# Kernel tuning notes

Hardware: AMD Instinct MI355X
Metric: run time of the kernel (lower is better)

Reference implementation:

```python
import jax, jax.numpy as jnp
import numpy as np

NX, NQ, NU, NY = 256, 256, 64, 64
EPS, ALPHA = 1e-3, 0.0
B = 32768


def setup_inputs() -> dict:
    key = jax.random.key(0)
    ks = jax.random.split(key, 8)
    std = np.float32(0.1 / np.sqrt(NX))
    return {
        "t": 0,
        "xi": jax.random.normal(ks[0], (B, NX), jnp.float32),
        "u": jax.random.normal(ks[1], (B, NU), jnp.float32),
        "Pstar": jax.random.normal(ks[2], (NX, NX), jnp.float32) * std,
        "Chi": jax.random.normal(ks[3], (NX, NQ), jnp.float32) * std,
        "Y1": jax.random.normal(ks[4], (NX, NX), jnp.float32) * std,
        "B2": jax.random.normal(ks[5], (NX, NU), jnp.float32) * std,
        "D12": jax.random.normal(ks[6], (NQ, NU), jnp.float32) * std,
        "X": jax.random.normal(ks[7], (NX + NQ, NX + NQ), jnp.float32) * std,
        "bx": jnp.zeros((NX,), jnp.float32),
        "bv": jnp.zeros((NQ,), jnp.float32),
    }


def _constrained_matrices(Pstar, Chi, Y1, X):
    # P = 0.5 Pstar Pstar^T + eps I ; H = X X^T + eps I
    P = 0.5 * (Pstar @ Pstar.T) + EPS * jnp.eye(NX, dtype=Pstar.dtype)
    H = X @ X.T + EPS * jnp.eye(NX + NQ, dtype=X.dtype)
    H1 = H[:NX, :NX]          # [nx,nx]
    H2 = H[:NX, NX:]          # [nx,nq]
    H4 = H[NX:, NX:]          # [nq,nq]
    Y = -0.5 * (H1 + ALPHA * P + Y1 - Y1.T)
    lam_inv = 1.0 / (0.5 * jnp.diagonal(H4))     # inverse of diagonal Lambda
    P_inv = jnp.linalg.inv(P)
    A = P_inv @ Y                                 # F.linear(P_inv, Y.T)
    D11 = -(lam_inv[:, None] * jnp.tril(H4, -1))  # strictly lower triangular [nq,nq]
    C1 = lam_inv[:, None] * Chi.T                 # [nq,nx]
    Z = -H2 - Chi
    B1 = P_inv @ Z                                # [nx,nq]
    return A, B1, C1, D11


def _compute_w(xi, u, C1, D11, D12, bv):
    # v_base[:, i] = xi @ C1[i] + u @ D12[i] + bv[i]  (all steps at once)
    v_base = xi @ C1.T + u @ D12.T + bv           # [B,nq]
    w0 = jnp.zeros_like(v_base)

    def step(w, i):
        # D11 row i is zero for j >= i, and w[:, j>=i] is still zero, so a full
        # matvec exactly reproduces the triangular forward substitution.
        v = v_base[:, i] + w @ D11[i]
        return w.at[:, i].set(jnp.tanh(v)), None

    w, _ = jax.lax.scan(step, w0, jnp.arange(NQ))
    return w


def reference(t, xi, u, Pstar, Chi, Y1, B2, D12, X, bx, bv):
    A, B1, C1, D11 = _constrained_matrices(Pstar, Chi, Y1, X)
    w = _compute_w(xi, u, C1, D11, D12, bv)       # [B,nq]
    xi_dot = xi @ A.T + w @ B1.T + u @ B2.T + bx  # [B,nx]
    return xi_dot
```

## Files before the change

### kernel.cpp

```cpp
#include <hip/hip_runtime.h>
#include <math.h>

#define NXC 256
#define NQC 256
#define NUC 64
#define NHC 512
#define BR  32768
#define EPSC 1e-3f
#define NAUG 768
#define CVTB 1536

typedef _Float16 h2_t __attribute__((ext_vector_type(2)));
typedef _Float16 f16x8 __attribute__((ext_vector_type(8)));
typedef float f32x4 __attribute__((ext_vector_type(4)));
union h2u { h2_t h; unsigned int u; };

__device__ __forceinline__ h2_t pk_f16(float a, float b) {
#if __has_builtin(__builtin_amdgcn_cvt_pkrtz)
  return __builtin_bit_cast(h2_t, __builtin_amdgcn_cvt_pkrtz(a, b));
#else
  h2_t r; r.x = (_Float16)a; r.y = (_Float16)b; return r;
#endif
}
__device__ __forceinline__ unsigned int pk_bits(float a, float b) { h2u x; x.h = pk_f16(a, b); return x.u; }
__device__ __forceinline__ h2_t b2h(unsigned int u) { h2u x; x.u = u; return x.h; }
__device__ __forceinline__ unsigned int h2b(h2_t v) { h2u x; x.h = v; return x.u; }

__device__ __forceinline__ float fdot2f(h2_t a, h2_t b, float c) {
#if __has_builtin(__builtin_amdgcn_fdot2)
  return __builtin_amdgcn_fdot2(a, b, c, false);
#else
  return c + (float)a.x * (float)b.x + (float)a.y * (float)b.y;
#endif
}

__device__ __forceinline__ float fast_tanh(float x) {
  float ax = fabsf(x);
  float e  = __expf(-2.0f * ax);
  float r  = __fdividef(1.0f - e, 1.0f + e);
  return copysignf(r, x);
}

__device__ __forceinline__ float fast_rcp(float x) {
#if __has_builtin(__builtin_amdgcn_rcpf)
  return __builtin_amdgcn_rcpf(x);
#else
  return 1.0f / x;
#endif
}

__device__ __forceinline__ void inv32_wave(float r[32], int ii) {
#pragma unroll
  for (int k = 0; k < 32; ++k) {
    float rk[32];
#pragma unroll
    for (int j = 0; j < 32; ++j) rk[j] = __shfl(r[j], k);
    float d = fast_rcp(rk[k]);
    float fik = r[k];
    if (ii == k) {
#pragma unroll
      for (int j = 0; j < 32; ++j) r[j] = (j == k) ? d : rk[j] * d;
    } else {
#pragma unroll
      for (int j = 0; j < 32; ++j) r[j] = (j == k) ? (-fik * d) : (r[j] - fik * (d * rk[j]));
    }
  }
}

__global__ __launch_bounds__(256) void syrk_mfma_kernel(const float* __restrict__ Xin,
                                                        const float* __restrict__ Pstar,
                                                        float* __restrict__ Hm,
                                                        float* __restrict__ Naug,
                                                        const float* __restrict__ xi,
                                                        const float* __restrict__ u,
                                                        _Float16* __restrict__ xi16,
                                                        _Float16* __restrict__ u16) {
  __shared__ _Float16 Alds[128][72];
  __shared__ _Float16 Blds[64][72];
  const int b = blockIdx.x, t = threadIdx.x;
  if (b >= 40) {
    const int nxi = BR * NXC / 8, ntot = nxi + BR * NUC / 8;
    int idx = (b - 40) * 256 + t;
    int stride = CVTB * 256;
    for (int i = idx; i < ntot; i += stride) {
      const float* s; _Float16* d; int j;
      if (i < nxi) { s = xi; d = xi16; j = i; } else { s = u; d = u16; j = i - nxi; }
      float4 a = ((const float4*)s)[(size_t)j * 2];
      float4 bb = ((const float4*)s)[(size_t)j * 2 + 1];
      uint4 o;
      o.x = pk_bits(a.x, a.y);  o.y = pk_bits(a.z, a.w);
      o.z = pk_bits(bb.x, bb.y); o.w = pk_bits(bb.z, bb.w);
      ((uint4*)d)[j] = o;
    }
    return;
  }
  const float* src; float* dst; int n, K; float scale; int rowbase, colbase;
  if (b < 32) { src = Xin;   dst = Hm;   n = NHC;  K = NHC; scale = 1.0f; rowbase = (b >> 3) * 128; colbase = (b & 7) * 64; }
  else { int b2 = b - 32; src = Pstar; dst = Naug; n = NAUG; K = NXC; scale = 0.5f; rowbase = (b2 >> 2) * 128; colbase = (b2 & 3) * 64; }
  const int r_a = t >> 1, h_a = t & 1;
  const int r_b = t >> 2, q_b = t & 3;
  const int lane = t & 63, wv = t >> 6;
  const int wm = wv >> 1, wn = wv & 1;
  const int l15 = lane & 15, l4 = lane >> 4;
  f32x4 acc[4][2] = {};
  for (int k0 = 0; k0 < K; k0 += 64) {
    uint4 av[4], bvv[2];
    {
      const float* p = src + (size_t)(rowbase + r_a) * K + k0 + h_a * 32;
#pragma unroll
      for (int m = 0; m < 4; m++) {
        float4 x0 = *(const float4*)(p + m * 8);
        float4 x1 = *(const float4*)(p + m * 8 + 4);
        uint4 pk;
        pk.x = pk_bits(x0.x, x0.y); pk.y = pk_bits(x0.z, x0.w);
        pk.z = pk_bits(x1.x, x1.y); pk.w = pk_bits(x1.z, x1.w);
        av[m] = pk;
      }
    }
    {
      const float* p = src + (size_t)(colbase + r_b) * K + k0 + q_b * 16;
      float4 x0 = *(const float4*)p,       x1 = *(const float4*)(p + 4);
      float4 x2 = *(const float4*)(p + 8), x3 = *(const float4*)(p + 12);
      bvv[0].x = pk_bits(x0.x, x0.y); bvv[0].y = pk_bits(x0.z, x0.w);
      bvv[0].z = pk_bits(x1.x, x1.y); bvv[0].w = pk_bits(x1.z, x1.w);
      bvv[1].x = pk_bits(x2.x, x2.y); bvv[1].y = pk_bits(x2.z, x2.w);
      bvv[1].z = pk_bits(x3.x, x3.y); bvv[1].w = pk_bits(x3.z, x3.w);
    }
    __syncthreads();
#pragma unroll
    for (int m = 0; m < 4; m++) *(uint4*)&Alds[r_a][h_a * 32 + m * 8] = av[m];
    *(uint4*)&Blds[r_b][q_b * 16]     = bvv[0];
    *(uint4*)&Blds[r_b][q_b * 16 + 8] = bvv[1];
    __syncthreads();
#pragma unroll
    for (int ks = 0; ks < 2; ks++) {
      f16x8 af[4], bf[2];
#pragma unroll
      for (int fm = 0; fm < 4; fm++)
        af[fm] = *(const f16x8*)&Alds[wm * 64 + fm * 16 + l15][ks * 32 + l4 * 8];
#pragma unroll
      for (int fn = 0; fn < 2; fn++)
        bf[fn] = *(const f16x8*)&Blds[wn * 32 + fn * 16 + l15][ks * 32 + l4 * 8];
#pragma unroll
      for (int fm = 0; fm < 4; fm++)
#pragma unroll
        for (int fn = 0; fn < 2; fn++)
          acc[fm][fn] = __builtin_amdgcn_mfma_f32_16x16x32_f16(af[fm], bf[fn], acc[fm][fn], 0, 0, 0);
    }
  }
#pragma unroll
  for (int fm = 0; fm < 4; fm++)
#pragma unroll
    for (int fn = 0; fn < 2; fn++) {
      int col = colbase + wn * 32 + fn * 16 + l15;
      f32x4 a = acc[fm][fn];
#pragma unroll
      for (int reg = 0; reg < 4; reg++) {
        int row = rowbase + wm * 64 + fm * 16 + l4 * 4 + reg;
        float val = scale * a[reg] + ((row == col) ? EPSC : 0.f);
        dst[(size_t)row * n + col] = val;
      }
    }
}

__global__ __launch_bounds__(256) void derive_kernel(const float* __restrict__ H,
                                                     const float* __restrict__ Y1,
                                                     const float* __restrict__ Chi,
                                                     const float* __restrict__ D12,
                                                     const float* __restrict__ B2,
                                                     float* __restrict__ Naug,
                                                     unsigned int* __restrict__ dpk_g,
                                                     _Float16* __restrict__ C1h,
                                                     _Float16* __restrict__ D12h,
                                                     _Float16* __restrict__ B2h) {
  int i = blockIdx.x, j = threadIdx.x;
  float li = 2.0f / H[(size_t)(NXC + i) * NHC + NXC + i];
  Naug[(size_t)i * NAUG + NXC + j]     = -0.5f * (H[(size_t)i * NHC + j] + Y1[i * NXC + j] - Y1[j * NXC + i]);
  C1h[i * NXC + j] = (_Float16)(li * Chi[j * NQC + i]);
  Naug[(size_t)i * NAUG + 2 * NXC + j] = -H[(size_t)i * NHC + NXC + j] - Chi[i * NQC + j];
  float dv = (j < i) ? (-li * H[(size_t)(NXC + i) * NHC + NXC + j]) : 0.f;
  float dhi = __shfl_xor(dv, 1);
  if ((j & 1) == 0) dpk_g[(size_t)(j >> 1) * NXC + i] = pk_bits(dv, dhi);
  if (j < NUC) {
    D12h[i * NUC + j] = (_Float16)D12[i * NUC + j];
    B2h[i * NUC + j]  = (_Float16)B2[i * NUC + j];
  }
}

__global__ __launch_bounds__(256) void gjstep_kernel(const float* __restrict__ Nin,
                                                     float* __restrict__ Nout,
                                                     _Float16* __restrict__ Ah,
                                                     _Float16* __restrict__ B1h,
                                                     int k0) {
  __shared__ float Dl[32][33];
  __shared__ float cfl[8][33];
  const int t = threadIdx.x;
  const int row0 = blockIdx.x * 8;
  const bool last = (k0 + 32 == NXC);
  if (t < 64) {
    const int ii = t & 31;
    float r[32];
#pragma unroll
    for (int j = 0; j < 32; ++j) r[j] = Nin[(size_t)(k0 + ii) * NAUG + k0 + j];
    inv32_wave(r, ii);
    if (t < 32) {
#pragma unroll
      for (int j = 0; j < 32; ++j) Dl[ii][j] = r[j];
    }
  }
  __syncthreads();
  {
    const int rr = t >> 5, s = t & 31;
    const int i = row0 + rr;
    float c;
    if (i >= k0 && i < k0 + 32) {
      c = Dl[i - k0][s];
    } else {
      float g = 0.f;
#pragma unroll
      for (int q = 0; q < 32; ++q) g = fmaf(Nin[(size_t)i * NAUG + k0 + q], Dl[q][s], g);
      c = -g;
    }
    cfl[rr][s] = c;
  }
  __syncthreads();
  const int rr = t >> 5;
  const int i = row0 + rr;
  const bool piv = (i >= k0 && i < k0 + 32);
  float cf[32];
#pragma unroll
  for (int s = 0; s < 32; ++s) cf[s] = cfl[rr][s];
  const int c40 = (k0 + 32) >> 2;
  for (int c4 = c40 + (t & 31); c4 < (NAUG >> 2); c4 += 32) {
    float4 acc;
    if (piv) { acc.x = 0.f; acc.y = 0.f; acc.z = 0.f; acc.w = 0.f; }
    else     { acc = *(const float4*)&Nin[(size_t)i * NAUG + c4 * 4]; }
#pragma unroll
    for (int s = 0; s < 32; ++s) {
      float4 pv = *(const float4*)&Nin[(size_t)(k0 + s) * NAUG + c4 * 4];
      acc.x = fmaf(cf[s], pv.x, acc.x);
      acc.y = fmaf(cf[s], pv.y, acc.y);
      acc.z = fmaf(cf[s], pv.z, acc.z);
      acc.w = fmaf(cf[s], pv.w, acc.w);
    }
    if (!last) {
      *(float4*)&Nout[(size_t)i * NAUG + c4 * 4] = acc;
    } else {
      int cc = c4 * 4 - NXC;
      h2_t h0, h1;
      h0.x = (_Float16)acc.x; h0.y = (_Float16)acc.y;
      h1.x = (_Float16)acc.z; h1.y = (_Float16)acc.w;
      uint2 o; o.x = h2b(h0); o.y = h2b(h1);
      if (cc < NXC) *(uint2*)&Ah[(size_t)i * NXC + cc]          = o;
      else          *(uint2*)&B1h[(size_t)i * NXC + (cc - NXC)] = o;
    }
  }
}

__global__ __launch_bounds__(256, 2) void wrec_fused_kernel(
    const _Float16* __restrict__ xi16, const _Float16* __restrict__ u16,
    const _Float16* __restrict__ C1h, const _Float16* __restrict__ D12h,
    const float* __restrict__ bv, const unsigned int* __restrict__ dpk_g,
    const _Float16* __restrict__ Ah, const _Float16* __restrict__ B1h,
    const _Float16* __restrict__ B2h, const float* __restrict__ bx,
    float* __restrict__ out) {
  __shared__ unsigned int pool[14976];
  unsigned int* wlds  = pool;
  unsigned int* dpkT  = pool + 8448;
  unsigned int* tript = pool + 12160;
  float*        vbuf  = (float*)(pool + 12672);

  const int t = threadIdx.x;
  const int r = t >> 2, s = t & 3;
  const int lane = t & 63, w = t >> 6;
  const int l15 = lane & 15, l4 = lane >> 4;
  const size_t rowbase = (size_t)blockIdx.x * 64;
  const _Float16* wl16 = (const _Float16*)wlds;

  f16x8 xi_frag[8], u_frag[2];
  {
    const _Float16* px = xi16 + (rowbase + w * 16 + l15) * NXC + l4 * 8;
#pragma unroll
    for (int kc = 0; kc < 8; ++kc) xi_frag[kc] = *(const f16x8*)(px + kc * 32);
    const _Float16* pu = u16 + (rowbase + w * 16 + l15) * NUC + l4 * 8;
#pragma unroll
    for (int kc = 0; kc < 2; ++kc) u_frag[kc] = *(const f16x8*)(pu + kc * 32);
  }

  h2_t wpk[16];
#pragma unroll
  for (int p = 0; p < 16; ++p) wpk[p] = pk_f16(0.f, 0.f);

  for (int kb = 0; kb < 8; ++kb) {
    const int i0 = kb * 32;
    for (int idx = t; idx < (i0 >> 1) * 32; idx += 256) {
      int cc = idx & 31, jp = idx >> 5;
      dpkT[cc * 116 + jp] = dpk_g[(size_t)jp * NXC + i0 + cc];
    }
    if (t < 128) {
      int jp = t >> 3, iq = t & 7;
      uint4 d4 = *(const uint4*)&dpk_g[(size_t)(i0 / 2 + jp) * NXC + i0 + iq * 4];
      tript[(iq * 4 + 0) * 16 + jp] = d4.x;
      tript[(iq * 4 + 1) * 16 + jp] = d4.y;
      tript[(iq * 4 + 2) * 16 + jp] = d4.z;
      tript[(iq * 4 + 3) * 16 + jp] = d4.w;
    }
    f32x4 acc0, acc1;
    {
      float b0 = bv[i0 + l15], b1 = bv[i0 + 16 + l15];
      acc0[0] = b0; acc0[1] = b0; acc0[2] = b0; acc0[3] = b0;
      acc1[0] = b1; acc1[1] = b1; acc1[2] = b1; acc1[3] = b1;
#pragma unroll
      for (int kc = 0; kc < 8; ++kc) {
        f16x8 bf0 = *(const f16x8*)&C1h[(size_t)(i0 + l15) * NXC + kc * 32 + l4 * 8];
        f16x8 bf1 = *(const f16x8*)&C1h[(size_t)(i0 + 16 + l15) * NXC + kc * 32 + l4 * 8];
        acc0 = __builtin_amdgcn_mfma_f32_16x16x32_f16(xi_frag[kc], bf0, acc0, 0, 0, 0);
        acc1 = __builtin_amdgcn_mfma_f32_16x16x32_f16(xi_frag[kc], bf1, acc1, 0, 0, 0);
      }
#pragma unroll
      for (int kc = 0; kc < 2; ++kc) {
        f16x8 bf0 = *(const f16x8*)&D12h[(size_t)(i0 + l15) * NUC + kc * 32 + l4 * 8];
        f16x8 bf1 = *(const f16x8*)&D12h[(size_t)(i0 + 16 + l15) * NUC + kc * 32 + l4 * 8];
        acc0 = __builtin_amdgcn_mfma_f32_16x16x32_f16(u_frag[kc], bf0, acc0, 0, 0, 0);
        acc1 = __builtin_amdgcn_mfma_f32_16x16x32_f16(u_frag[kc], bf1, acc1, 0, 0, 0);
      }
    }
    __syncthreads();

    for (int ks = 0; ks < kb; ++ks) {
      f16x8 af = *(const f16x8*)&wl16[(size_t)(w * 16 + l15) * 264 + ks * 32 + l4 * 8];
      uint4 b0 = *(const uint4*)&dpkT[(l15) * 116 + ks * 16 + l4 * 4];
      uint4 b1 = *(const uint4*)&dpkT[(16 + l15) * 116 + ks * 16 + l4 * 4];
      acc0 = __builtin_amdgcn_mfma_f32_16x16x32_f16(af, __builtin_bit_cast(f16x8, b0), acc0, 0, 0, 0);
      acc1 = __builtin_amdgcn_mfma_f32_16x16x32_f16(af, __builtin_bit_cast(f16x8, b1), acc1, 0, 0, 0);
    }

#pragma unroll
    for (int reg = 0; reg < 4; ++reg) {
      int rowm = w * 16 + l4 * 4 + reg;
      vbuf[rowm * 36 + l15]      = acc0[reg];
      vbuf[rowm * 36 + 16 + l15] = acc1[reg];
    }

    float wprev = 0.f;
#pragma unroll
    for (int i = 0; i < 32; ++i) {
      const int npairs = (i + 1) >> 1;
      const int nq = (npairs + 3) >> 2;
      float td0 = 0.f, td1 = 0.f;
#pragma unroll
      for (int q = 0; q < nq; ++q) {
        uint4 tq = *(const uint4*)&tript[i * 16 + q * 4];
        td0 = fdot2f(wpk[q * 4 + 0], b2h(tq.x), td0);
        td1 = fdot2f(wpk[q * 4 + 1], b2h(tq.y), td1);
        td0 = fdot2f(wpk[q * 4 + 2], b2h(tq.z), td0);
        td1 = fdot2f(wpk[q * 4 + 3], b2h(tq.w), td1);
      }
      float vi = vbuf[r * 36 + i];
      float wi = fast_tanh(vi + td0 + td1);
      if ((i & 1) == 0) { wprev = wi; wpk[i >> 1] = pk_f16(wi, 0.f); }
      else              { wpk[i >> 1] = pk_f16(wprev, wi); }
    }

    {
      uint4 o;
      o.x = h2b(wpk[s * 4 + 0]); o.y = h2b(wpk[s * 4 + 1]);
      o.z = h2b(wpk[s * 4 + 2]); o.w = h2b(wpk[s * 4 + 3]);
      *(uint4*)&wlds[r * 132 + kb * 16 + s * 4] = o;
    }
    __syncthreads();
  }

  _Float16* Ws = (_Float16*)dpkT;
  f32x4 oacc[16];
#pragma unroll
  for (int ct = 0; ct < 16; ++ct) {
    float bb = bx[ct * 16 + l15];
    oacc[ct][0] = bb; oacc[ct][1] = bb; oacc[ct][2] = bb; oacc[ct][3] = bb;
  }
  uint4 pa, pb, pc, pd;
  {
    const _Float16* p = Ah + (size_t)t * NXC;
    pa = *(const uint4*)p;        pb = *(const uint4*)(p + 8);
    pc = *(const uint4*)(p + 16); pd = *(const uint4*)(p + 24);
  }
#pragma unroll
  for (int rr = 0; rr < 18; ++rr) {
    const int sel = rr < 8 ? 0 : (rr < 16 ? 1 : 2);
    const int kc  = sel == 0 ? rr : (sel == 1 ? rr - 8 : rr - 16);
    __syncthreads();
    *(uint4*)&Ws[t * 40]      = pa;
    *(uint4*)&Ws[t * 40 + 8]  = pb;
    *(uint4*)&Ws[t * 40 + 16] = pc;
    *(uint4*)&Ws[t * 40 + 24] = pd;
    __syncthreads();
    if (rr < 17) {
      const int rs = rr + 1;
      const int s2 = rs < 8 ? 0 : (rs < 16 ? 1 : 2);
      const int k2 = s2 == 0 ? rs : (s2 == 1 ? rs - 8 : rs - 16);
      const _Float16* Wp = s2 == 0 ? Ah : (s2 == 1 ? B1h : B2h);
      const int KK = (s2 == 2) ? NUC : NXC;
      const _Float16* p = Wp + (size_t)t * KK + k2 * 32;
      pa = *(const uint4*)p;        pb = *(const uint4*)(p + 8);
      pc = *(const uint4*)(p + 16); pd = *(const uint4*)(p + 24);
    }
    f16x8 af;
    if (sel == 0)      af = xi_frag[kc];
    else if (sel == 1) af = *(const f16x8*)&wl16[(size_t)(w * 16 + l15) * 264 + kc * 32 + l4 * 8];
    else               af = u_frag[kc];
#pragma unroll
    for (int ct = 0; ct < 16; ++ct) {
      f16x8 bf = *(const f16x8*)&Ws[(ct * 16 + l15) * 40 + l4 * 8];
      oacc[ct] = __builtin_amdgcn_mfma_f32_16x16x32_f16(af, bf, oacc[ct], 0, 0, 0);
    }
  }
#pragma unroll
  for (int ct = 0; ct < 16; ++ct) {
#pragma unroll
    for (int reg = 0; reg < 4; ++reg) {
      int row = (int)rowbase + w * 16 + l4 * 4 + reg;
      out[(size_t)row * NXC + ct * 16 + l15] = oacc[ct][reg];
    }
  }
}

extern "C" void kernel_launch(void* const* d_in, const int* in_sizes, int n_in,
                              void* d_out, int out_size, void* d_ws, size_t ws_size,
                              hipStream_t stream) {
  (void)in_sizes; (void)n_in; (void)out_size; (void)ws_size;
  const float* xi    = (const float*)d_in[1];
  const float* u     = (const float*)d_in[2];
  const float* Pstar = (const float*)d_in[3];
  const float* Chi   = (const float*)d_in[4];
  const float* Y1    = (const float*)d_in[5];
  const float* B2    = (const float*)d_in[6];
  const float* D12   = (const float*)d_in[7];
  const float* Xin   = (const float*)d_in[8];
  const float* bx    = (const float*)d_in[9];
  const float* bv    = (const float*)d_in[10];
  float* out = (float*)d_out;

  float* ws = (float*)d_ws;
  _Float16* xi16 = (_Float16*)ws;
  _Float16* u16  = xi16 + (size_t)BR * NXC;
  float* Hm = (float*)(u16 + (size_t)BR * NUC);
  float* NA = Hm + (size_t)NHC * NHC;
  float* NB = NA + (size_t)NXC * NAUG;
  unsigned int* dpkg = (unsigned int*)(NB + (size_t)NXC * NAUG);
  _Float16* C1h  = (_Float16*)(dpkg + 128 * 256);
  _Float16* D12h = C1h + (size_t)NQC * NXC;
  _Float16* Ah   = D12h + (size_t)NQC * NUC;
  _Float16* B1h  = Ah + (size_t)NXC * NXC;
  _Float16* B2h  = B1h + (size_t)NXC * NQC;

  syrk_mfma_kernel<<<40 + CVTB, 256, 0, stream>>>(Xin, Pstar, Hm, NA, xi, u, xi16, u16);
  derive_kernel<<<NXC, NXC, 0, stream>>>(Hm, Y1, Chi, D12, B2, NA, dpkg, C1h, D12h, B2h);

  for (int kb = 0; kb < 8; ++kb) {
    const float* Nin = (kb & 1) ? NB : NA;
    float*      Nout = (kb & 1) ? NA : NB;
    gjstep_kernel<<<32, 256, 0, stream>>>(Nin, Nout, Ah, B1h, kb * 32);
  }

  wrec_fused_kernel<<<BR / 64, 256, 0, stream>>>(
      xi16, u16, C1h, D12h, bv, dpkg, Ah, B1h, B2h, bx, out);
}
```

Before: 305.1 us.

## Fuse Gauss-Jordan inversion steps into recurrence kernel with atomic cross-block sync

Drops the eight separate gjstep kernel launches. The first 32 blocks of the recurrence kernel now run the Gauss-Jordan steps in between their own w-recurrence stages, and an atomic counter plus spin-waits orders the steps across blocks. Every block waits for the counter to finish before the final output GEMM that reads A and B1. This removes launch gaps and overlaps the matrix inversion with the recurrence. The cost is extra shared memory, spin-wait stalls in the first blocks, and a possible deadlock if those 32 blocks are not all resident at the same time.

```diff
diff --git a/kernel.cpp b/kernel.cpp
--- a/kernel.cpp
+++ b/kernel.cpp
@@ -172,8 +172,10 @@
                                                      unsigned int* __restrict__ dpk_g,
                                                      _Float16* __restrict__ C1h,
                                                      _Float16* __restrict__ D12h,
-                                                     _Float16* __restrict__ B2h) {
+                                                     _Float16* __restrict__ B2h,
+                                                     unsigned int* gjc) {
   int i = blockIdx.x, j = threadIdx.x;
+  if (i == 0 && j == 0) *gjc = 0u;
   float li = 2.0f / H[(size_t)(NXC + i) * NHC + NXC + i];
   Naug[(size_t)i * NAUG + NXC + j]     = -0.5f * (H[(size_t)i * NHC + j] + Y1[i * NXC + j] - Y1[j * NXC + i]);
   C1h[i * NXC + j] = (_Float16)(li * Chi[j * NQC + i]);
@@ -187,15 +189,12 @@
   }
 }
 
-__global__ __launch_bounds__(256) void gjstep_kernel(const float* __restrict__ Nin,
-                                                     float* __restrict__ Nout,
-                                                     _Float16* __restrict__ Ah,
-                                                     _Float16* __restrict__ B1h,
-                                                     int k0) {
-  __shared__ float Dl[32][33];
-  __shared__ float cfl[8][33];
-  const int t = threadIdx.x;
-  const int row0 = blockIdx.x * 8;
+__device__ __forceinline__ void gj_step(const float* __restrict__ Nin,
+                                        float* __restrict__ Nout,
+                                        _Float16* __restrict__ Ah,
+                                        _Float16* __restrict__ B1h,
+                                        int k0, int row0, int t,
+                                        float (*Dl)[33], float (*cfl)[33]) {
   const bool last = (k0 + 32 == NXC);
   if (t < 64) {
     const int ii = t & 31;
@@ -261,10 +260,13 @@
     const _Float16* __restrict__ xi16, const _Float16* __restrict__ u16,
     const _Float16* __restrict__ C1h, const _Float16* __restrict__ D12h,
     const float* __restrict__ bv, const unsigned int* __restrict__ dpk_g,
-    const _Float16* __restrict__ Ah, const _Float16* __restrict__ B1h,
+    _Float16* __restrict__ Ah, _Float16* __restrict__ B1h,
     const _Float16* __restrict__ B2h, const float* __restrict__ bx,
-    float* __restrict__ out) {
+    float* __restrict__ out,
+    float* __restrict__ NA, float* __restrict__ NB, unsigned int* gjc) {
   __shared__ unsigned int pool[14976];
+  __shared__ float Dl[32][33];
+  __shared__ float cfl[8][33];
   unsigned int* wlds  = pool;
   unsigned int* dpkT  = pool + 8448;
   unsigned int* tript = pool + 12160;
@@ -292,6 +294,23 @@
   for (int p = 0; p < 16; ++p) wpk[p] = pk_f16(0.f, 0.f);
 
   for (int kb = 0; kb < 8; ++kb) {
+    if (blockIdx.x < 32) {
+      if (kb > 0) {
+        if (t == 0) {
+          while (__hip_atomic_load(gjc, __ATOMIC_ACQUIRE, __HIP_MEMORY_SCOPE_AGENT) < 32u * (unsigned)kb)
+            __builtin_amdgcn_s_sleep(8);
+        }
+        __syncthreads();
+        __threadfence();
+      }
+      const float* Nin = (kb & 1) ? NB : NA;
+      float*      Nout = (kb & 1) ? NA : NB;
+      gj_step(Nin, Nout, Ah, B1h, kb * 32, blockIdx.x * 8, t, Dl, cfl);
+      __threadfence();
+      __syncthreads();
+      if (t == 0) __hip_atomic_fetch_add(gjc, 1u, __ATOMIC_RELEASE, __HIP_MEMORY_SCOPE_AGENT);
+    }
+
     const int i0 = kb * 32;
     for (int idx = t; idx < (i0 >> 1) * 32; idx += 256) {
       int cc = idx & 31, jp = idx >> 5;
@@ -370,6 +389,13 @@
     }
     __syncthreads();
   }
+
+  if (t == 0) {
+    while (__hip_atomic_load(gjc, __ATOMIC_ACQUIRE, __HIP_MEMORY_SCOPE_AGENT) < 256u)
+      __builtin_amdgcn_s_sleep(8);
+  }
+  __syncthreads();
+  __threadfence();
 
   _Float16* Ws = (_Float16*)dpkT;
   f32x4 oacc[16];
@@ -452,16 +478,11 @@
   _Float16* Ah   = D12h + (size_t)NQC * NUC;
   _Float16* B1h  = Ah + (size_t)NXC * NXC;
   _Float16* B2h  = B1h + (size_t)NXC * NQC;
+  unsigned int* gjc = (unsigned int*)(B2h + (size_t)NXC * NUC);
 
   syrk_mfma_kernel<<<40 + CVTB, 256, 0, stream>>>(Xin, Pstar, Hm, NA, xi, u, xi16, u16);
-  derive_kernel<<<NXC, NXC, 0, stream>>>(Hm, Y1, Chi, D12, B2, NA, dpkg, C1h, D12h, B2h);
-
-  for (int kb = 0; kb < 8; ++kb) {
-    const float* Nin = (kb & 1) ? NB : NA;
-    float*      Nout = (kb & 1) ? NA : NB;
-    gjstep_kernel<<<32, 256, 0, stream>>>(Nin, Nout, Ah, B1h, kb * 32);
-  }
+  derive_kernel<<<NXC, NXC, 0, stream>>>(Hm, Y1, Chi, D12, B2, NA, dpkg, C1h, D12h, B2h, gjc);
 
   wrec_fused_kernel<<<BR / 64, 256, 0, stream>>>(
-      xi16, u16, C1h, D12h, bv, dpkg, Ah, B1h, B2h, bx, out);
-}
+      xi16, u16, C1h, D12h, bv, dpkg, Ah, B1h, B2h, bx, out, NA, NB, gjc);
+}
```

Result: slower. 1.037 ms (+239.8%).
